# Kernel tuning notes

Hardware: AMD Instinct MI355X
Metric: run time of the kernel (lower is better)

Reference implementation:

```python
import jax, jax.numpy as jnp
import numpy as np

B, N = 4, 8192
D = 128
DEPTH = 4
LEAF = 32
HEADS = 4
HD = D // HEADS
SLOTS = 24
RANKS = [20, 32, 52, 82]                      # rank at encoder step j (fine -> coarse)
EXP = [RANKS[j] * (2 ** j) for j in range(DEPTH)]  # HODLR head output dims


def _rope_tables(seq_len, dim):
    inv_freq = 1.0 / (10000.0 ** (jnp.arange(0, dim, 2, dtype=jnp.float32) / dim))
    t = jnp.arange(seq_len, dtype=jnp.float32)
    freqs = t[:, None] * inv_freq[None, :]
    emb = jnp.concatenate([freqs, freqs], axis=-1)   # [S, dim]
    return jnp.cos(emb), jnp.sin(emb)


def _rotate_half(x):
    x1, x2 = jnp.split(x, 2, axis=-1)
    return jnp.concatenate([-x2, x1], axis=-1)


def _layernorm(x, g, b, eps=1e-5):
    mu = jnp.mean(x, -1, keepdims=True)
    var = jnp.mean((x - mu) ** 2, -1, keepdims=True)
    return (x - mu) * jax.lax.rsqrt(var + eps) * g + b


def _block_attn(h, qkv_w, qkv_b, pw, pb, cos, sin):
    Bc, Nc, C = h.shape
    nb = Nc // LEAF
    xb = h.reshape(Bc * nb, LEAF, C)
    qkv = (xb @ qkv_w + qkv_b).reshape(Bc * nb, LEAF, 3, HEADS, HD)
    qkv = qkv.transpose(2, 0, 3, 1, 4)               # [3, BN, H, L, hd]
    q, k, v = qkv[0], qkv[1], qkv[2]
    q = q * cos + _rotate_half(q) * sin              # full-dim RoPE (rope_dim == head_dim)
    k = k * cos + _rotate_half(k) * sin
    attn = jax.nn.softmax(jnp.einsum('bhqd,bhkd->bhqk', q, k) * (HD ** -0.5), axis=-1)
    o = jnp.einsum('bhqk,bhkd->bhqd', attn, v).transpose(0, 2, 1, 3).reshape(Bc * nb, LEAF, C)
    return (o @ pw + pb).reshape(Bc, Nc, C)


def _forward(x, cen_w, cen_b, nbr_w, nbr_b, inp_w, inp_b,
             leafp_w, leafp_b, leafh_w, leafh_b, log_scale_leaf,
             ln1_g, ln1_b, qkv_w, qkv_b, attnp_w, attnp_b,
             ln2_g, ln2_b, mlp1_w, mlp1_b, mlp2_w, mlp2_b, ds_w, ds_b,
             hu_w0, hu_b0, hv_w0, hv_b0, hu_w1, hu_b1, hv_w1, hv_b1,
             hu_w2, hu_b2, hv_w2, hv_b2, hu_w3, hu_b3, hv_w3, hv_b3):
    Bx, Nx, _ = x.shape
    # --- SymmetricNeighborEmbed (24 neighbor slots, vectorized) ---
    pos_i = x[..., 0:3]
    diag_i = x[..., 3:4]
    h_center = jnp.concatenate([pos_i, diag_i], -1) @ cen_w + cen_b          # [B,N,D]
    nb_feat = x[..., 4:4 + 5 * SLOTS].reshape(Bx, Nx, SLOTS, 5)
    rel = nb_feat[..., 0:1]
    pos_j = nb_feat[..., 1:4]
    w_ij = nb_feat[..., 4:5]
    active = (w_ij != 0.0).astype(x.dtype)
    feat = jnp.concatenate([rel * active, (pos_j - pos_i[:, :, None, :]) * active, w_ij], -1)
    e = (feat @ nbr_w + nbr_b) * active                                       # [B,N,24,D]
    h = h_center + jnp.sum(e, axis=2)
    h = h @ inp_w + inp_b
    # --- leaf dense diagonal blocks ---
    nl = Nx // LEAF
    hl = h.reshape(Bx, nl, LEAF, D) @ leafp_w + leafp_b                       # [B,nl,32,32]
    u_leaf = hl @ leafh_w + leafh_b
    dense = jnp.einsum('blik,bljk->blij', u_leaf, u_leaf) * jnp.exp(log_scale_leaf)
    diag_a = x[..., 3]                                                        # scale_A defaults to 1.0
    mask = jnp.abs(diag_a) > 1e-6
    new_diag = jnp.where(mask, 1.0 / jnp.where(mask, diag_a, 1.0), 1.0).reshape(Bx, nl, LEAF)
    dense = dense + new_diag[..., :, None] * jnp.eye(LEAF, dtype=x.dtype)
    # --- down-only encoder: transformer block -> HODLR head -> 2:1 downsample ---
    cos, sin = _rope_tables(LEAF, HD)
    hu = [(hu_w0, hu_b0), (hu_w1, hu_b1), (hu_w2, hu_b2), (hu_w3, hu_b3)]
    hv = [(hv_w0, hv_b0), (hv_w1, hv_b1), (hv_w2, hv_b2), (hv_w3, hv_b3)]
    us, vs = [], []
    for j in range(DEPTH):
        a = _block_attn(_layernorm(h, ln1_g[j], ln1_b[j]),
                        qkv_w[j], qkv_b[j], attnp_w[j], attnp_b[j], cos, sin)
        h = h + a
        m = _layernorm(h, ln2_g[j], ln2_b[j])
        m = jax.nn.gelu(m @ mlp1_w[j] + mlp1_b[j], approximate=False) @ mlp2_w[j] + mlp2_b[j]
        h = h + m
        us.append((h @ hu[j][0] + hu[j][1]).reshape(Bx, Nx, RANKS[j]))
        vs.append((h @ hv[j][0] + hv[j][1]).reshape(Bx, Nx, RANKS[j]))
        Bh, n, c = h.shape
        h = h.reshape(Bh, n // 2, 2 * c) @ ds_w[j] + ds_b[j]
    # single flat output: dense leaf blocks + all U/V HODLR factors
    return jnp.concatenate([dense.reshape(Bx, -1),
                            jnp.concatenate(us, -1).reshape(Bx, -1),
                            jnp.concatenate(vs, -1).reshape(Bx, -1)], -1)


def setup_inputs():
    key = jax.random.key(0)
    ks = iter(jax.random.split(key, 64))
    def rn(shape, s=0.05):
        return jax.random.normal(next(ks), shape, jnp.float32) * s
    z = lambda *s: jnp.zeros(s, jnp.float32)
    o = lambda *s: jnp.ones(s, jnp.float32)
    inp = {
        'x': jax.random.normal(next(ks), (B, N, 4 + 5 * SLOTS), jnp.float32),
        'cen_w': rn((4, D)), 'cen_b': z(D),
        'nbr_w': rn((5, D)), 'nbr_b': z(D),
        'inp_w': rn((D, D)), 'inp_b': z(D),
        'leafp_w': rn((D, LEAF)), 'leafp_b': z(LEAF),
        'leafh_w': rn((LEAF, LEAF), 0.01), 'leafh_b': z(LEAF),
        'log_scale_leaf': jnp.full((1,), np.log(0.01), jnp.float32),
        'ln1_g': o(DEPTH, D), 'ln1_b': z(DEPTH, D),
        'qkv_w': rn((DEPTH, D, 3 * D)), 'qkv_b': z(DEPTH, 3 * D),
        'attnp_w': rn((DEPTH, D, D)), 'attnp_b': z(DEPTH, D),
        'ln2_g': o(DEPTH, D), 'ln2_b': z(DEPTH, D),
        'mlp1_w': rn((DEPTH, D, 4 * D)), 'mlp1_b': z(DEPTH, 4 * D),
        'mlp2_w': rn((DEPTH, 4 * D, D)), 'mlp2_b': z(DEPTH, D),
        'ds_w': rn((DEPTH, 2 * D, D)), 'ds_b': z(DEPTH, D),
    }
    for j in range(DEPTH):
        inp['hu_w%d' % j] = rn((D, EXP[j]), 0.01)
        inp['hu_b%d' % j] = z(EXP[j])
        inp['hv_w%d' % j] = rn((D, EXP[j]), 0.01)
        inp['hv_b%d' % j] = z(EXP[j])
    return inp


def reference(x, cen_w, cen_b, nbr_w, nbr_b, inp_w, inp_b,
              leafp_w, leafp_b, leafh_w, leafh_b, log_scale_leaf,
              ln1_g, ln1_b, qkv_w, qkv_b, attnp_w, attnp_b,
              ln2_g, ln2_b, mlp1_w, mlp1_b, mlp2_w, mlp2_b, ds_w, ds_b,
              hu_w0, hu_b0, hv_w0, hv_b0, hu_w1, hu_b1, hv_w1, hv_b1,
              hu_w2, hu_b2, hv_w2, hv_b2, hu_w3, hu_b3, hv_w3, hv_b3):
    return _forward(x, cen_w, cen_b, nbr_w, nbr_b, inp_w, inp_b,
                    leafp_w, leafp_b, leafh_w, leafh_b, log_scale_leaf,
                    ln1_g, ln1_b, qkv_w, qkv_b, attnp_w, attnp_b,
                    ln2_g, ln2_b, mlp1_w, mlp1_b, mlp2_w, mlp2_b, ds_w, ds_b,
                    hu_w0, hu_b0, hv_w0, hv_b0, hu_w1, hu_b1, hv_w1, hv_b1,
                    hu_w2, hu_b2, hv_w2, hv_b2, hu_w3, hu_b3, hv_w3, hv_b3)
```

## Files before the change

### kernel.cpp

```cpp
#include <hip/hip_runtime.h>
#include <math.h>

#define DEV __device__ __forceinline__

constexpr int XFv = 124;
constexpr size_t OPB   = 3309568;
constexpr size_t UBASE = 262144;
constexpr size_t VBASE = 1785856;
constexpr int UVWID = 186;

using bfrag  = __attribute__((ext_vector_type(8))) short;
using f32x4v = __attribute__((ext_vector_type(4))) float;

DEV float* at4p(float* base, int t, int c0, int W) {
  return base + t * W + ((c0 + 4 * t) & (W - 1));
}
DEV float& at1r(float* base, int t, int c, int W) {
  return base[t * W + (((c & ~3) + 4 * t) & (W - 1)) + (c & 3)];
}
DEV float4 ld4g(const float* p) { return *(const float4*)p; }
DEV void fma4(float4& a, float s, const float4& w) {
  a.x += s * w.x; a.y += s * w.y; a.z += s * w.z; a.w += s * w.w;
}
DEV float gelu_fast(float x) {
  float x2 = x * x;
  float z = x * (1.5957691216057308f + 0.0713551f * x2);
  float e = __expf(z);
  float r = 1.0f - __frcp_rn(e + 1.0f);
  return x * r;
}
DEV ushort f2bf(float x) {
  unsigned u = __float_as_uint(x);
  unsigned r = (u + 0x7fffu + ((u >> 16) & 1u)) >> 16;
  return (ushort)r;
}
DEV void stb128(ushort* b, int row, int col, float v) {
  b[row * 128 + (((col & ~7) + 8 * row) & 127) + (col & 7)] = f2bf(v);
}

__global__ __launch_bounds__(256) void wprep_all_kernel(
    const float* __restrict__ src0, ushort* __restrict__ dst0, int K, int N) {
  size_t off = (size_t)blockIdx.z * K * N;
  const float* src = src0 + off;
  ushort* dst = dst0 + off;
  __shared__ float S[64][65];
  int tid = threadIdx.x;
  int k0 = blockIdx.x * 64, n0 = blockIdx.y * 64;
  for (int i = tid; i < 64 * 64; i += 256) {
    int kk = i >> 6, nn = i & 63;
    S[kk][nn] = src[(size_t)(k0 + kk) * N + n0 + nn];
  }
  __syncthreads();
  int n = tid >> 2, kq = tid & 3;
  unsigned pk[8];
#pragma unroll
  for (int i = 0; i < 8; i++) {
    int k = kq * 16 + 2 * i;
    pk[i] = (unsigned)f2bf(S[k][n]) | ((unsigned)f2bf(S[k + 1][n]) << 16);
  }
  unsigned* dp = (unsigned*)&dst[(size_t)(n0 + n) * K + k0 + kq * 16];
#pragma unroll
  for (int i = 0; i < 8; i++) dp[i] = pk[i];
}

struct UVDesc {
  const float* src[8];
  ushort* dst[8];
  int expj[8];
  int npad[8];
};
__global__ __launch_bounds__(256) void uvprep_all_kernel(UVDesc d) {
  int mi = blockIdx.y;
  int i = blockIdx.x * 256 + threadIdx.x;
  int expj = d.expj[mi];
  if (i >= d.npad[mi] * 128) return;
  int n = i >> 7, k = i & 127;
  d.dst[mi][(size_t)n * 128 + k] =
      (n < expj) ? f2bf(d.src[mi][(size_t)k * expj + n]) : (ushort)0;
}

__global__ __launch_bounds__(128) void weff_prep_kernel(
    const float* __restrict__ cw, const float* __restrict__ cb,
    const float* __restrict__ nw, const float* __restrict__ nb,
    const float* __restrict__ iw, const float* __restrict__ ib,
    float* __restrict__ weff, float* __restrict__ ropetab) {
  __shared__ float S[11 * 128];
  int tid = threadIdx.x;
  for (int i = tid; i < 512; i += 128) S[i] = cw[i];
  for (int i = tid; i < 640; i += 128) S[512 + i] = nw[i];
  S[1152 + tid] = nb[tid];
  S[1280 + tid] = cb[tid];
  __syncthreads();
  float acc[11];
#pragma unroll
  for (int r = 0; r < 10; r++) acc[r] = 0.f;
  acc[10] = ib[tid];
  for (int k = 0; k < 128; k++) {
    float w = iw[k * 128 + tid];
#pragma unroll
    for (int r = 0; r < 11; r++) acc[r] += S[r * 128 + k] * w;
  }
#pragma unroll
  for (int r = 0; r < 11; r++) weff[r * 128 + tid] = acc[r];
  for (int idx = tid; idx < 512; idx += 128) {
    int pos = idx >> 4, d = idx & 15;
    float ang = (float)pos * expf(-0.57564627324851148f * (float)d);
    ropetab[idx] = cosf(ang);
    ropetab[512 + idx] = sinf(ang);
  }
}

__global__ __launch_bounds__(256) void node_embed2_kernel(
    const float* __restrict__ x, const float* __restrict__ weff,
    float* __restrict__ h) {
  __shared__ float XR[64 * XFv];
  __shared__ float RF[64][11];
  __shared__ __align__(16) float WE[11 * 128];
  int tid = threadIdx.x;
  int node0 = blockIdx.x * 64;
  for (int i = tid; i < 64 * XFv; i += 256)
    XR[i] = x[(size_t)node0 * XFv + i];
  for (int i = tid; i < 11 * 128; i += 256) WE[i] = weff[i];
  __syncthreads();
  {
    int nn = tid >> 2, sl = tid & 3;
    const float* xr = XR + nn * XFv;
    float p0 = xr[0], p1 = xr[1], p2 = xr[2];
    float g[6] = {0.f, 0.f, 0.f, 0.f, 0.f, 0.f};
#pragma unroll
    for (int s = 0; s < 6; s++) {
      const float* f = xr + 4 + 5 * (sl * 6 + s);
      float w = f[4];
      if (w != 0.0f) {
        g[0] += f[0]; g[1] += f[1] - p0; g[2] += f[2] - p1;
        g[3] += f[3] - p2; g[4] += w; g[5] += 1.0f;
      }
    }
#pragma unroll
    for (int i = 0; i < 6; i++) {
      g[i] += __shfl_xor(g[i], 1);
      g[i] += __shfl_xor(g[i], 2);
    }
    if (sl == 0) {
      RF[nn][0] = p0; RF[nn][1] = p1; RF[nn][2] = p2; RF[nn][3] = xr[3];
#pragma unroll
      for (int i = 0; i < 6; i++) RF[nn][4 + i] = g[i];
    }
  }
  __syncthreads();
  {
    int w = tid >> 6, lane = tid & 63;
    int c4 = lane & 31, hi = lane >> 5;
    const float4* WE4 = (const float4*)WE;
#pragma unroll
    for (int rr = 0; rr < 8; rr++) {
      int node = w * 16 + rr * 2 + hi;
      float4 acc = WE4[10 * 32 + c4];
#pragma unroll
      for (int f = 0; f < 10; f++)
        fma4(acc, RF[node][f], WE4[f * 32 + c4]);
      *(float4*)&h[(size_t)(node0 + node) * 128 + c4 * 4] = acc;
    }
  }
}

__global__ __launch_bounds__(256) void leaf_dense_kernel(
    const float* __restrict__ h, const float* __restrict__ x,
    const float* __restrict__ lpw, const float* __restrict__ lpb,
    const float* __restrict__ lhw, const float* __restrict__ lhb,
    const float* __restrict__ lsc, float* __restrict__ out) {
  __shared__ __align__(16) float HS[32 * 128];
  __shared__ __align__(16) float HL[32 * 32];
  __shared__ __align__(16) float UL[32 * 32];
  int tid = threadIdx.x;
  int leaf = blockIdx.x;
  size_t base = (size_t)leaf * (32 * 128);
  for (int i = tid; i < 32 * 128; i += 256) {
    int t = i >> 7, c = i & 127;
    at1r(HS, t, c, 128) = h[base + i];
  }
  __syncthreads();
  int t = tid & 31, cg = tid >> 5;
  {
    float4 acc = ld4g(&lpb[4 * cg]);
    for (int k4 = 0; k4 < 128; k4 += 4) {
      float4 xv = *(const float4*)at4p(HS, t, k4, 128);
      float xa[4] = {xv.x, xv.y, xv.z, xv.w};
#pragma unroll
      for (int kk = 0; kk < 4; kk++)
        fma4(acc, xa[kk], ld4g(&lpw[(k4 + kk) * 32 + 4 * cg]));
    }
    *(float4*)at4p(HL, t, 4 * cg, 32) = acc;
  }
  __syncthreads();
  {
    float4 acc = ld4g(&lhb[4 * cg]);
    for (int k4 = 0; k4 < 32; k4 += 4) {
      float4 xv = *(const float4*)at4p(HL, t, k4, 32);
      float xa[4] = {xv.x, xv.y, xv.z, xv.w};
#pragma unroll
      for (int kk = 0; kk < 4; kk++)
        fma4(acc, xa[kk], ld4g(&lhw[(k4 + kk) * 32 + 4 * cg]));
    }
    *(float4*)at4p(UL, t, 4 * cg, 32) = acc;
  }
  __syncthreads();
  {
    float scale = expf(lsc[0]);
    float acc[4] = {0.f, 0.f, 0.f, 0.f};
    for (int k4 = 0; k4 < 32; k4 += 4) {
      float4 xv = *(const float4*)at4p(UL, t, k4, 32);
      float xa[4] = {xv.x, xv.y, xv.z, xv.w};
#pragma unroll
      for (int kk = 0; kk < 4; kk++) {
        int k = k4 + kk;
#pragma unroll
        for (int i2 = 0; i2 < 4; i2++)
          acc[i2] += xa[kk] * at1r(UL, 4 * cg + i2, k, 32);
      }
    }
    int b = leaf >> 8, l = leaf & 255;
#pragma unroll
    for (int i2 = 0; i2 < 4; i2++) {
      int c = 4 * cg + i2;
      float v = acc[i2] * scale;
      if (c == t) {
        float dg = x[(size_t)(leaf * 32 + t) * XFv + 3];
        v += (fabsf(dg) > 1e-6f) ? (1.0f / dg) : 1.0f;
      }
      out[(size_t)b * OPB + (size_t)l * 1024 + t * 32 + c] = v;
    }
  }
}

__global__ __launch_bounds__(256) void layer_mfma_kernel(
    float* __restrict__ h,
    const float* __restrict__ lng, const float* __restrict__ lnb,
    const ushort* __restrict__ wqkvt, const float* __restrict__ bqkv,
    const ushort* __restrict__ wpt, const float* __restrict__ pb,
    const float* __restrict__ rt,
    const float* __restrict__ ln2g, const float* __restrict__ ln2b,
    const ushort* __restrict__ w1t, const float* __restrict__ b1,
    const ushort* __restrict__ w2t, const float* __restrict__ b2) {
  __shared__ __align__(16) ushort SM[32768];
  ushort* XN = SM;
  ushort* QB = SM + 8192;
  ushort* KB = SM + 16384;
  ushort* VT = SM + 24576;
  float*  HS = (float*)(SM + 16384);
  int tid = threadIdx.x;
  size_t base = (size_t)blockIdx.x * (64 * 128);

  {
    int m = tid >> 2, p = tid & 3;
    const float* row = h + base + m * 128 + p * 32;
    float v[32];
    float s = 0.f;
#pragma unroll
    for (int i = 0; i < 32; i += 4) {
      float4 t4 = ld4g(row + i);
      v[i] = t4.x; v[i + 1] = t4.y; v[i + 2] = t4.z; v[i + 3] = t4.w;
      s += t4.x + t4.y + t4.z + t4.w;
    }
    s += __shfl_xor(s, 1); s += __shfl_xor(s, 2);
    float mu = s * (1.0f / 128.0f);
    float s2 = 0.f;
#pragma unroll
    for (int i = 0; i < 32; i++) { float d = v[i] - mu; s2 += d * d; }
    s2 += __shfl_xor(s2, 1); s2 += __shfl_xor(s2, 2);
    float rs = rsqrtf(s2 * (1.0f / 128.0f) + 1e-5f);
    unsigned* XW = (unsigned*)XN;
#pragma unroll
    for (int i = 0; i < 32; i += 2) {
      int c = p * 32 + i;
      float x0 = (v[i] - mu) * rs * lng[c] + lnb[c];
      float x1 = (v[i + 1] - mu) * rs * lng[c + 1] + lnb[c + 1];
      int kp = c >> 1;
      XW[m * 64 + ((kp + 4 * m) & 63)] =
          (unsigned)f2bf(x0) | ((unsigned)f2bf(x1) << 16);
    }
  }
  __syncthreads();

  int w = tid >> 6, l = tid & 63, lm = l & 15, q = l >> 4;

  {
    f32x4v acc[4][6];
#pragma unroll
    for (int mt = 0; mt < 4; mt++)
#pragma unroll
      for (int nt = 0; nt < 6; nt++) acc[mt][nt] = (f32x4v){0.f, 0.f, 0.f, 0.f};
    for (int ks = 0; ks < 4; ks++) {
      bfrag a[4];
#pragma unroll
      for (int mt = 0; mt < 4; mt++) {
        int mm = mt * 16 + lm;
        a[mt] = *(const bfrag*)&XN[mm * 128 + ((ks * 32 + q * 8 + 8 * mm) & 127)];
      }
#pragma unroll
      for (int nt = 0; nt < 6; nt++) {
        int n = w * 96 + nt * 16 + lm;
        bfrag b = *(const bfrag*)&wqkvt[(size_t)n * 128 + ks * 32 + q * 8];
#pragma unroll
        for (int mt = 0; mt < 4; mt++)
          acc[mt][nt] = __builtin_amdgcn_mfma_f32_16x16x32_bf16(
              a[mt], b, acc[mt][nt], 0, 0, 0);
      }
    }
    float csA[4] = {}, snA[4] = {}, csB[4] = {}, snB[4] = {};
    if (w < 3) {
#pragma unroll
      for (int r = 0; r < 4; r++) {
        int pa = q * 4 + r;
        csA[r] = rt[pa * 16 + lm];        snA[r] = rt[512 + pa * 16 + lm];
        csB[r] = rt[(pa + 16) * 16 + lm]; snB[r] = rt[512 + (pa + 16) * 16 + lm];
      }
    }
#pragma unroll
    for (int p2 = 0; p2 < 3; p2++) {
      int g = w * 6 + 2 * p2;
      int ne = g * 16 + lm;
      if (g < 16) {
        float be = bqkv[ne], bo = bqkv[ne + 16];
        ushort* dst = (g < 8) ? QB : KB;
        int de = (g < 8) ? ne : ne - 128;
#pragma unroll
        for (int mt = 0; mt < 4; mt++)
#pragma unroll
          for (int r = 0; r < 4; r++) {
            int mm = mt * 16 + q * 4 + r;
            float cs = (mt & 1) ? csB[r] : csA[r];
            float sn = (mt & 1) ? snB[r] : snA[r];
            float e = acc[mt][2 * p2][r] + be;
            float o = acc[mt][2 * p2 + 1][r] + bo;
            stb128(dst, mm, de, e * cs - o * sn);
            stb128(dst, mm, de + 16, o * cs + e * sn);
          }
      } else {
#pragma unroll
        for (int h2 = 0; h2 < 2; h2++) {
          int nt = 2 * p2 + h2;
          int nv = (g + h2) * 16 + lm;
          int dv = nv - 256;
          float bv = bqkv[nv];
#pragma unroll
          for (int mt = 0; mt < 4; mt++) {
            int t0 = mt * 16 + q * 4;
            short4 pk;
            pk.x = (short)f2bf(acc[mt][nt][0] + bv);
            pk.y = (short)f2bf(acc[mt][nt][1] + bv);
            pk.z = (short)f2bf(acc[mt][nt][2] + bv);
            pk.w = (short)f2bf(acc[mt][nt][3] + bv);
            *(short4*)&VT[dv * 64 + (((t0 & ~7) + 8 * dv) & 63) + (t0 & 7)] = pk;
          }
        }
      }
    }
  }
  __syncthreads();

  ushort* SP = XN;
  {
#pragma unroll
    for (int ci = 0; ci < 2; ci++) {
      int combo = w + 4 * ci;
      int head = combo >> 1, leaf = combo & 1;
      f32x4v sc[2][2];
#pragma unroll
      for (int a2 = 0; a2 < 2; a2++)
#pragma unroll
        for (int b2 = 0; b2 < 2; b2++) sc[a2][b2] = (f32x4v){0.f, 0.f, 0.f, 0.f};
      bfrag qa[2], kb[2];
#pragma unroll
      for (int mt2 = 0; mt2 < 2; mt2++) {
        int row = leaf * 32 + mt2 * 16 + lm;
        qa[mt2] = *(const bfrag*)&QB[row * 128 + ((head * 32 + q * 8 + 8 * row) & 127)];
      }
#pragma unroll
      for (int nt2 = 0; nt2 < 2; nt2++) {
        int kt = leaf * 32 + nt2 * 16 + lm;
        kb[nt2] = *(const bfrag*)&KB[kt * 128 + ((head * 32 + q * 8 + 8 * kt) & 127)];
      }
#pragma unroll
      for (int mt2 = 0; mt2 < 2; mt2++)
#pragma unroll
        for (int nt2 = 0; nt2 < 2; nt2++)
          sc[mt2][nt2] = __builtin_amdgcn_mfma_f32_16x16x32_bf16(
              qa[mt2], kb[nt2], sc[mt2][nt2], 0, 0, 0);
      const float scl = 0.17677669529663688f;
#pragma unroll
      for (int mt2 = 0; mt2 < 2; mt2++)
#pragma unroll
        for (int nt2 = 0; nt2 < 2; nt2++)
#pragma unroll
          for (int r = 0; r < 4; r++) {
            int qt = leaf * 32 + mt2 * 16 + q * 4 + r;
            int kc = nt2 * 16 + lm;
            SP[head * 2048 + qt * 32 + (((kc & ~7) + 8 * qt) & 31) + (kc & 7)] =
                f2bf(sc[mt2][nt2][r] * scl);
          }
    }
  }
  __syncthreads();

  {
    int head = tid >> 6, qt = tid & 63;
    ushort* rowp = SP + head * 2048 + qt * 32;
    float v[32];
#pragma unroll
    for (int pc = 0; pc < 4; pc++) {
      uint4 ch = *(const uint4*)&rowp[pc * 8];
      unsigned uu[4] = {ch.x, ch.y, ch.z, ch.w};
#pragma unroll
      for (int i2 = 0; i2 < 4; i2++) {
        v[pc * 8 + 2 * i2]     = __uint_as_float(uu[i2] << 16);
        v[pc * 8 + 2 * i2 + 1] = __uint_as_float(uu[i2] & 0xffff0000u);
      }
    }
    float mx = -1e30f;
#pragma unroll
    for (int i = 0; i < 32; i++) mx = fmaxf(mx, v[i]);
    float s = 0.f;
#pragma unroll
    for (int i = 0; i < 32; i++) { v[i] = __expf(v[i] - mx); s += v[i]; }
    float inv = 1.0f / s;
#pragma unroll
    for (int pc = 0; pc < 4; pc++) {
      uint4 ch;
      unsigned uu[4];
#pragma unroll
      for (int i2 = 0; i2 < 4; i2++)
        uu[i2] = (unsigned)f2bf(v[pc * 8 + 2 * i2] * inv) |
                 ((unsigned)f2bf(v[pc * 8 + 2 * i2 + 1] * inv) << 16);
      ch.x = uu[0]; ch.y = uu[1]; ch.z = uu[2]; ch.w = uu[3];
      *(uint4*)&rowp[pc * 8] = ch;
    }
  }
  __syncthreads();

  ushort* OB = QB;
  {
#pragma unroll
    for (int ci = 0; ci < 2; ci++) {
      int combo = w + 4 * ci;
      int head = combo >> 1, leaf = combo & 1;
      f32x4v ov[2][2];
#pragma unroll
      for (int a2 = 0; a2 < 2; a2++)
#pragma unroll
        for (int b2 = 0; b2 < 2; b2++) ov[a2][b2] = (f32x4v){0.f, 0.f, 0.f, 0.f};
      bfrag pa[2], vb[2];
#pragma unroll
      for (int mt2 = 0; mt2 < 2; mt2++) {
        int qt = leaf * 32 + mt2 * 16 + lm;
        pa[mt2] = *(const bfrag*)&SP[head * 2048 + qt * 32 + ((q * 8 + 8 * qt) & 31)];
      }
#pragma unroll
      for (int nt2 = 0; nt2 < 2; nt2++) {
        int gdim = head * 32 + nt2 * 16 + lm;
        int t0 = leaf * 32 + q * 8;
        vb[nt2] = *(const bfrag*)&VT[gdim * 64 + ((t0 + 8 * gdim) & 63)];
      }
#pragma unroll
      for (int mt2 = 0; mt2 < 2; mt2++)
#pragma unroll
        for (int nt2 = 0; nt2 < 2; nt2++)
          ov[mt2][nt2] = __builtin_amdgcn_mfma_f32_16x16x32_bf16(
              pa[mt2], vb[nt2], ov[mt2][nt2], 0, 0, 0);
#pragma unroll
      for (int mt2 = 0; mt2 < 2; mt2++)
#pragma unroll
        for (int nt2 = 0; nt2 < 2; nt2++)
#pragma unroll
          for (int r = 0; r < 4; r++) {
            int qt = leaf * 32 + mt2 * 16 + q * 4 + r;
            int gdim = head * 32 + nt2 * 16 + lm;
            stb128(OB, qt, gdim, ov[mt2][nt2][r]);
          }
    }
  }
  __syncthreads();

  {
    f32x4v po[4][2];
#pragma unroll
    for (int mt = 0; mt < 4; mt++)
#pragma unroll
      for (int nt = 0; nt < 2; nt++) po[mt][nt] = (f32x4v){0.f, 0.f, 0.f, 0.f};
    for (int ks = 0; ks < 4; ks++) {
      bfrag a[4];
#pragma unroll
      for (int mt = 0; mt < 4; mt++) {
        int mm = mt * 16 + lm;
        a[mt] = *(const bfrag*)&OB[mm * 128 + ((ks * 32 + q * 8 + 8 * mm) & 127)];
      }
#pragma unroll
      for (int nt = 0; nt < 2; nt++) {
        int n = w * 32 + nt * 16 + lm;
        bfrag b = *(const bfrag*)&wpt[(size_t)n * 128 + ks * 32 + q * 8];
#pragma unroll
        for (int mt = 0; mt < 4; mt++)
          po[mt][nt] = __builtin_amdgcn_mfma_f32_16x16x32_bf16(
              a[mt], b, po[mt][nt], 0, 0, 0);
      }
    }
#pragma unroll
    for (int nt = 0; nt < 2; nt++) {
      int n = w * 32 + nt * 16 + lm;
      float bv = pb[n];
#pragma unroll
      for (int mt = 0; mt < 4; mt++)
#pragma unroll
        for (int r = 0; r < 4; r++) {
          int mm = mt * 16 + q * 4 + r;
          HS[mm * 128 + n] = po[mt][nt][r] + bv;
        }
    }
  }
  __syncthreads();

  {
    int j = tid & 31;
    int c0 = j * 4;
    float g0 = ln2g[c0], g1 = ln2g[c0 + 1], g2 = ln2g[c0 + 2], g3 = ln2g[c0 + 3];
    float e0 = ln2b[c0], e1 = ln2b[c0 + 1], e2 = ln2b[c0 + 2], e3 = ln2b[c0 + 3];
    unsigned* XW = (unsigned*)XN;
#pragma unroll
    for (int k2 = 0; k2 < 8; k2++) {
      int idx = tid + 256 * k2;
      int tok = idx >> 5;
      float4 hg = ld4g(&h[base + (size_t)idx * 4]);
      float4 ao = *(const float4*)&HS[idx * 4];
      float4 hn;
      hn.x = hg.x + ao.x; hn.y = hg.y + ao.y;
      hn.z = hg.z + ao.z; hn.w = hg.w + ao.w;
      *(float4*)&HS[idx * 4] = hn;
      float s = hn.x + hn.y + hn.z + hn.w;
      s += __shfl_xor(s, 1); s += __shfl_xor(s, 2); s += __shfl_xor(s, 4);
      s += __shfl_xor(s, 8); s += __shfl_xor(s, 16);
      float mu = s * (1.0f / 128.0f);
      float d0 = hn.x - mu, d1 = hn.y - mu, d2 = hn.z - mu, d3 = hn.w - mu;
      float s2 = d0 * d0 + d1 * d1 + d2 * d2 + d3 * d3;
      s2 += __shfl_xor(s2, 1); s2 += __shfl_xor(s2, 2); s2 += __shfl_xor(s2, 4);
      s2 += __shfl_xor(s2, 8); s2 += __shfl_xor(s2, 16);
      float rs = rsqrtf(s2 * (1.0f / 128.0f) + 1e-5f);
      float x0 = d0 * rs * g0 + e0;
      float x1 = d1 * rs * g1 + e1;
      float x2 = d2 * rs * g2 + e2;
      float x3 = d3 * rs * g3 + e3;
      int kp = 2 * j;
      XW[tok * 64 + ((kp + 4 * tok) & 63)] =
          (unsigned)f2bf(x0) | ((unsigned)f2bf(x1) << 16);
      XW[tok * 64 + ((kp + 1 + 4 * tok) & 63)] =
          (unsigned)f2bf(x2) | ((unsigned)f2bf(x3) << 16);
    }
  }
  __syncthreads();

  ushort* HC = QB;
  f32x4v acc2[4][2];
#pragma unroll
  for (int mt = 0; mt < 4; mt++)
#pragma unroll
    for (int nt = 0; nt < 2; nt++) acc2[mt][nt] = (f32x4v){0.f, 0.f, 0.f, 0.f};

  for (int hc = 0; hc < 4; hc++) {
    f32x4v acc1[4][2];
#pragma unroll
    for (int mt = 0; mt < 4; mt++)
#pragma unroll
      for (int nt = 0; nt < 2; nt++) acc1[mt][nt] = (f32x4v){0.f, 0.f, 0.f, 0.f};
#pragma unroll
    for (int ks = 0; ks < 4; ks++) {
      bfrag a[4];
#pragma unroll
      for (int mt = 0; mt < 4; mt++) {
        int mm = mt * 16 + lm;
        a[mt] = *(const bfrag*)&XN[mm * 128 + ((ks * 32 + q * 8 + 8 * mm) & 127)];
      }
#pragma unroll
      for (int nt = 0; nt < 2; nt++) {
        int n = hc * 128 + w * 32 + nt * 16 + lm;
        bfrag b = *(const bfrag*)&w1t[(size_t)n * 128 + ks * 32 + q * 8];
#pragma unroll
        for (int mt = 0; mt < 4; mt++)
          acc1[mt][nt] = __builtin_amdgcn_mfma_f32_16x16x32_bf16(
              a[mt], b, acc1[mt][nt], 0, 0, 0);
      }
    }
    if (hc) __syncthreads();
#pragma unroll
    for (int nt = 0; nt < 2; nt++) {
      int nl = w * 32 + nt * 16 + lm;
      float b1v = b1[hc * 128 + nl];
#pragma unroll
      for (int mt = 0; mt < 4; mt++)
#pragma unroll
        for (int r = 0; r < 4; r++) {
          int mm = mt * 16 + q * 4 + r;
          float val = gelu_fast(acc1[mt][nt][r] + b1v);
          HC[mm * 128 + (((nl & ~7) + 8 * mm) & 127) + (nl & 7)] = f2bf(val);
        }
    }
    __syncthreads();
#pragma unroll
    for (int ks = 0; ks < 4; ks++) {
      bfrag a[4];
#pragma unroll
      for (int mt = 0; mt < 4; mt++) {
        int mm = mt * 16 + lm;
        a[mt] = *(const bfrag*)&HC[mm * 128 + ((ks * 32 + q * 8 + 8 * mm) & 127)];
      }
#pragma unroll
      for (int nt = 0; nt < 2; nt++) {
        int n = w * 32 + nt * 16 + lm;
        bfrag b = *(const bfrag*)&w2t[(size_t)n * 512 + hc * 128 + ks * 32 + q * 8];
#pragma unroll
        for (int mt = 0; mt < 4; mt++)
          acc2[mt][nt] = __builtin_amdgcn_mfma_f32_16x16x32_bf16(
              a[mt], b, acc2[mt][nt], 0, 0, 0);
      }
    }
  }

#pragma unroll
  for (int nt = 0; nt < 2; nt++) {
    int n = w * 32 + nt * 16 + lm;
    float b2v = b2[n];
#pragma unroll
    for (int mt = 0; mt < 4; mt++)
#pragma unroll
      for (int r = 0; r < 4; r++) {
        int mm = mt * 16 + q * 4 + r;
        h[base + (size_t)mm * 128 + n] = HS[mm * 128 + n] + acc2[mt][nt][r] + b2v;
      }
  }
}

template <int EXPJ, int RANK, int LVL, int NSPLIT>
__global__ __launch_bounds__(256) void uv_mfma_kernel(
    const float* __restrict__ h,
    const ushort* __restrict__ uwt, const float* __restrict__ ub,
    const ushort* __restrict__ vwt, const float* __restrict__ vb,
    float* __restrict__ out, int Nj) {
  constexpr int NT16 = (EXPJ + 15) / 16;
  constexpr int NJOBS = 2 * NT16;
  constexpr int COFF = (LVL == 0) ? 0 : (LVL == 1) ? 20 : (LVL == 2) ? 52 : 104;
  __shared__ __align__(16) ushort XN[64 * 128];
  int tid = threadIdx.x;
  int t0 = blockIdx.x * 64;
  size_t base = (size_t)t0 * 128;
  {
    int m = tid >> 2, p = tid & 3;
    const float* row = h + base + m * 128 + p * 32;
    unsigned* XW = (unsigned*)XN;
#pragma unroll
    for (int i = 0; i < 32; i += 4) {
      float4 t4 = ld4g(row + i);
      int kp = (p * 32 + i) >> 1;
      XW[m * 64 + ((kp + 4 * m) & 63)] =
          (unsigned)f2bf(t4.x) | ((unsigned)f2bf(t4.y) << 16);
      XW[m * 64 + ((kp + 1 + 4 * m) & 63)] =
          (unsigned)f2bf(t4.z) | ((unsigned)f2bf(t4.w) << 16);
    }
  }
  __syncthreads();
  int bidx = t0 / Nj;
  int tl0 = t0 - bidx * Nj;
  size_t obase = (size_t)bidx * OPB;
  int w = tid >> 6, l = tid & 63, lm = l & 15, q = l >> 4;
  int gw = w + 4 * blockIdx.y;
  for (int jj = gw; jj < NJOBS; jj += 4 * NSPLIT) {
    int uvsel = jj & 1, nt = jj >> 1;
    const ushort* wt = uvsel ? vwt : uwt;
    const float* bias = uvsel ? vb : ub;
    size_t ob = obase + (uvsel ? VBASE : UBASE);
    f32x4v acc[4];
#pragma unroll
    for (int mt = 0; mt < 4; mt++) acc[mt] = (f32x4v){0.f, 0.f, 0.f, 0.f};
    for (int ks = 0; ks < 4; ks++) {
      bfrag b = *(const bfrag*)&wt[(size_t)(nt * 16 + lm) * 128 + ks * 32 + q * 8];
#pragma unroll
      for (int mt = 0; mt < 4; mt++) {
        int mm = mt * 16 + lm;
        int ke = ks * 32 + q * 8;
        bfrag a = *(const bfrag*)&XN[mm * 128 + ((ke + 8 * mm) & 127)];
        acc[mt] = __builtin_amdgcn_mfma_f32_16x16x32_bf16(a, b, acc[mt], 0, 0, 0);
      }
    }
    int c = nt * 16 + lm;
    if (c < EXPJ) {
      float bv = bias[c];
      int cdiv = c / RANK, cmod = c - cdiv * RANK;
#pragma unroll
      for (int mt = 0; mt < 4; mt++)
#pragma unroll
        for (int r = 0; r < 4; r++) {
          int mm = mt * 16 + q * 4 + r;
          int nrow = ((tl0 + mm) << LVL) + cdiv;
          out[ob + (size_t)nrow * UVWID + COFF + cmod] = acc[mt][r] + bv;
        }
    }
  }
}

__global__ __launch_bounds__(256) void ds_mfma_kernel(
    const float* __restrict__ hin, float* __restrict__ hout,
    const ushort* __restrict__ wt, const float* __restrict__ bias) {
  __shared__ __align__(16) ushort XN[64 * 256];
  int tid = threadIdx.x;
  size_t base = (size_t)blockIdx.x * (64 * 256);
  {
    int m = tid >> 2, p = tid & 3;
    const float* row = hin + base + m * 256 + p * 64;
    unsigned* XW = (unsigned*)XN;
#pragma unroll
    for (int i = 0; i < 64; i += 4) {
      float4 t4 = ld4g(row + i);
      int kp = (p * 64 + i) >> 1;
      XW[m * 128 + ((kp + 4 * m) & 127)] =
          (unsigned)f2bf(t4.x) | ((unsigned)f2bf(t4.y) << 16);
      XW[m * 128 + ((kp + 1 + 4 * m) & 127)] =
          (unsigned)f2bf(t4.z) | ((unsigned)f2bf(t4.w) << 16);
    }
  }
  __syncthreads();
  int w = tid >> 6, l = tid & 63, lm = l & 15, q = l >> 4;
  f32x4v acc[4][2];
#pragma unroll
  for (int mt = 0; mt < 4; mt++)
#pragma unroll
    for (int nt = 0; nt < 2; nt++) acc[mt][nt] = (f32x4v){0.f, 0.f, 0.f, 0.f};
  for (int ks = 0; ks < 8; ks++) {
    bfrag a[4];
#pragma unroll
    for (int mt = 0; mt < 4; mt++) {
      int mm = mt * 16 + lm;
      a[mt] = *(const bfrag*)&XN[mm * 256 + ((ks * 32 + q * 8 + 8 * mm) & 255)];
    }
#pragma unroll
    for (int nt = 0; nt < 2; nt++) {
      int n = w * 32 + nt * 16 + lm;
      bfrag b = *(const bfrag*)&wt[(size_t)n * 256 + ks * 32 + q * 8];
#pragma unroll
      for (int mt = 0; mt < 4; mt++)
        acc[mt][nt] = __builtin_amdgcn_mfma_f32_16x16x32_bf16(
            a[mt], b, acc[mt][nt], 0, 0, 0);
    }
  }
  size_t obase = (size_t)blockIdx.x * (64 * 128);
#pragma unroll
  for (int nt = 0; nt < 2; nt++) {
    int n = w * 32 + nt * 16 + lm;
    float bv = bias[n];
#pragma unroll
    for (int mt = 0; mt < 4; mt++)
#pragma unroll
      for (int r = 0; r < 4; r++) {
        int mm = mt * 16 + q * 4 + r;
        hout[obase + (size_t)mm * 128 + n] = acc[mt][nt][r] + bv;
      }
  }
}

extern "C" void kernel_launch(void* const* d_in, const int* in_sizes, int n_in,
                              void* d_out, int out_size, void* d_ws, size_t ws_size,
                              hipStream_t stream) {
  const float* x       = (const float*)d_in[0];
  const float* cen_w   = (const float*)d_in[1];
  const float* cen_b   = (const float*)d_in[2];
  const float* nbr_w   = (const float*)d_in[3];
  const float* nbr_b   = (const float*)d_in[4];
  const float* inp_w   = (const float*)d_in[5];
  const float* inp_b   = (const float*)d_in[6];
  const float* leafp_w = (const float*)d_in[7];
  const float* leafp_b = (const float*)d_in[8];
  const float* leafh_w = (const float*)d_in[9];
  const float* leafh_b = (const float*)d_in[10];
  const float* lscale  = (const float*)d_in[11];
  const float* ln1_g   = (const float*)d_in[12];
  const float* ln1_b   = (const float*)d_in[13];
  const float* qkv_w   = (const float*)d_in[14];
  const float* qkv_b   = (const float*)d_in[15];
  const float* attnp_w = (const float*)d_in[16];
  const float* attnp_b = (const float*)d_in[17];
  const float* ln2_g   = (const float*)d_in[18];
  const float* ln2_b   = (const float*)d_in[19];
  const float* mlp1_w  = (const float*)d_in[20];
  const float* mlp1_b  = (const float*)d_in[21];
  const float* mlp2_w  = (const float*)d_in[22];
  const float* mlp2_b  = (const float*)d_in[23];
  const float* ds_w    = (const float*)d_in[24];
  const float* ds_b    = (const float*)d_in[25];
  const float* huw[4], *hub[4], *hvw[4], *hvb[4];
  for (int j = 0; j < 4; j++) {
    huw[j] = (const float*)d_in[26 + 4 * j];
    hub[j] = (const float*)d_in[27 + 4 * j];
    hvw[j] = (const float*)d_in[28 + 4 * j];
    hvb[j] = (const float*)d_in[29 + 4 * j];
  }
  float* out = (float*)d_out;
  float* hA = (float*)d_ws;
  float* hB = hA + (size_t)4 * 8192 * 128;
  ushort* w1t = (ushort*)(hB + (size_t)2097152);
  ushort* w2t = w1t + (size_t)4 * 65536;
  ushort* uvt = w2t + (size_t)4 * 65536;
  const int NPAD[4] = {32, 64, 208, 656};
  ushort* uwt[4]; ushort* vwt[4];
  ushort* p = uvt;
  for (int j = 0; j < 4; j++) {
    uwt[j] = p; p += (size_t)NPAD[j] * 128;
    vwt[j] = p; p += (size_t)NPAD[j] * 128;
  }
  ushort* wqkvt = p;
  ushort* wpt   = wqkvt + (size_t)4 * 384 * 128;
  ushort* dswt  = wpt + (size_t)4 * 128 * 128;
  float* weff   = (float*)(dswt + (size_t)4 * 128 * 256);
  float* ropetab = weff + 1408;
  const int EXPJ_[4] = {20, 64, 208, 656};

  weff_prep_kernel<<<1, 128, 0, stream>>>(
      cen_w, cen_b, nbr_w, nbr_b, inp_w, inp_b, weff, ropetab);
  wprep_all_kernel<<<dim3(2, 8, 4), 256, 0, stream>>>(mlp1_w, w1t, 128, 512);
  wprep_all_kernel<<<dim3(8, 2, 4), 256, 0, stream>>>(mlp2_w, w2t, 512, 128);
  wprep_all_kernel<<<dim3(2, 6, 4), 256, 0, stream>>>(qkv_w, wqkvt, 128, 384);
  wprep_all_kernel<<<dim3(2, 2, 4), 256, 0, stream>>>(attnp_w, wpt, 128, 128);
  wprep_all_kernel<<<dim3(4, 2, 4), 256, 0, stream>>>(ds_w, dswt, 256, 128);
  {
    UVDesc d;
    for (int j = 0; j < 4; j++) {
      d.src[2 * j] = huw[j];     d.dst[2 * j] = uwt[j];
      d.src[2 * j + 1] = hvw[j]; d.dst[2 * j + 1] = vwt[j];
      d.expj[2 * j] = EXPJ_[j];  d.expj[2 * j + 1] = EXPJ_[j];
      d.npad[2 * j] = NPAD[j];   d.npad[2 * j + 1] = NPAD[j];
    }
    uvprep_all_kernel<<<dim3(328, 8), 256, 0, stream>>>(d);
  }

  node_embed2_kernel<<<(4 * 8192) / 64, 256, 0, stream>>>(x, weff, hA);
  leaf_dense_kernel<<<(4 * 8192) / 32, 256, 0, stream>>>(
      hA, x, leafp_w, leafp_b, leafh_w, leafh_b, lscale, out);

  float* cur = hA;
  float* nxt = hB;
  int Nj = 8192;
  for (int j = 0; j < 4; j++) {
    int tokens = 4 * Nj;
    layer_mfma_kernel<<<tokens / 64, 256, 0, stream>>>(
        cur, ln1_g + j * 128, ln1_b + j * 128,
        wqkvt + (size_t)j * 49152, qkv_b + j * 384,
        wpt + (size_t)j * 16384, attnp_b + j * 128, ropetab,
        ln2_g + j * 128, ln2_b + j * 128,
        w1t + (size_t)j * 65536, mlp1_b + j * 512,
        w2t + (size_t)j * 65536, mlp2_b + j * 128);
    if (j == 0)
      uv_mfma_kernel<20, 20, 0, 1><<<dim3(tokens / 64, 1), 256, 0, stream>>>(
          cur, uwt[0], hub[0], vwt[0], hvb[0], out, Nj);
    else if (j == 1)
      uv_mfma_kernel<64, 32, 1, 2><<<dim3(tokens / 64, 2), 256, 0, stream>>>(
          cur, uwt[1], hub[1], vwt[1], hvb[1], out, Nj);
    else if (j == 2)
      uv_mfma_kernel<208, 52, 2, 4><<<dim3(tokens / 64, 4), 256, 0, stream>>>(
          cur, uwt[2], hub[2], vwt[2], hvb[2], out, Nj);
    else
      uv_mfma_kernel<656, 82, 3, 8><<<dim3(tokens / 64, 8), 256, 0, stream>>>(
          cur, uwt[3], hub[3], vwt[3], hvb[3], out, Nj);
    ds_mfma_kernel<<<tokens / 128, 256, 0, stream>>>(
        cur, nxt, dswt + (size_t)j * 32768, ds_b + j * 128);
    float* tmp = cur; cur = nxt; nxt = tmp;
    Nj >>= 1;
  }
  (void)in_sizes; (void)n_in; (void)out_size; (void)ws_size;
}
```

Measured before the change: 470.4 us.

## Shrink layer kernel tile to 32 tokens per block for higher occupancy

Each layer_mfma_kernel block now processes one 32-token leaf instead of two, halving shared memory (64KB to 32KB) and accumulator registers, and requests 4 blocks per CU via launch bounds. Attention is remapped so each wave handles one head of the single leaf, and only half the threads run the softmax. The HS fp32 scratch now uses a swizzled layout to reduce LDS bank conflicts. In exchange, weight fragments are reloaded from global/L2 twice as often per token, and the grid doubles.

```diff
diff --git a/kernel.cpp b/kernel.cpp
--- a/kernel.cpp
+++ b/kernel.cpp
@@ -233,7 +233,7 @@
   }
 }
 
-__global__ __launch_bounds__(256) void layer_mfma_kernel(
+__global__ __launch_bounds__(256, 4) void layer_mfma_kernel(
     float* __restrict__ h,
     const float* __restrict__ lng, const float* __restrict__ lnb,
     const ushort* __restrict__ wqkvt, const float* __restrict__ bqkv,
@@ -242,37 +242,37 @@
     const float* __restrict__ ln2g, const float* __restrict__ ln2b,
     const ushort* __restrict__ w1t, const float* __restrict__ b1,
     const ushort* __restrict__ w2t, const float* __restrict__ b2) {
-  __shared__ __align__(16) ushort SM[32768];
+  __shared__ __align__(16) ushort SM[16384];
   ushort* XN = SM;
-  ushort* QB = SM + 8192;
-  ushort* KB = SM + 16384;
-  ushort* VT = SM + 24576;
-  float*  HS = (float*)(SM + 16384);
+  ushort* QB = SM + 4096;
+  ushort* KB = SM + 8192;
+  ushort* VT = SM + 12288;
+  float*  HS = (float*)(SM + 8192);
   int tid = threadIdx.x;
-  size_t base = (size_t)blockIdx.x * (64 * 128);
-
-  {
-    int m = tid >> 2, p = tid & 3;
-    const float* row = h + base + m * 128 + p * 32;
-    float v[32];
+  size_t base = (size_t)blockIdx.x * (32 * 128);
+
+  {
+    int m = tid >> 3, p = tid & 7;
+    const float* row = h + base + m * 128 + p * 16;
+    float v[16];
     float s = 0.f;
 #pragma unroll
-    for (int i = 0; i < 32; i += 4) {
+    for (int i = 0; i < 16; i += 4) {
       float4 t4 = ld4g(row + i);
       v[i] = t4.x; v[i + 1] = t4.y; v[i + 2] = t4.z; v[i + 3] = t4.w;
       s += t4.x + t4.y + t4.z + t4.w;
     }
-    s += __shfl_xor(s, 1); s += __shfl_xor(s, 2);
+    s += __shfl_xor(s, 1); s += __shfl_xor(s, 2); s += __shfl_xor(s, 4);
     float mu = s * (1.0f / 128.0f);
     float s2 = 0.f;
 #pragma unroll
-    for (int i = 0; i < 32; i++) { float d = v[i] - mu; s2 += d * d; }
-    s2 += __shfl_xor(s2, 1); s2 += __shfl_xor(s2, 2);
+    for (int i = 0; i < 16; i++) { float d = v[i] - mu; s2 += d * d; }
+    s2 += __shfl_xor(s2, 1); s2 += __shfl_xor(s2, 2); s2 += __shfl_xor(s2, 4);
     float rs = rsqrtf(s2 * (1.0f / 128.0f) + 1e-5f);
     unsigned* XW = (unsigned*)XN;
 #pragma unroll
-    for (int i = 0; i < 32; i += 2) {
-      int c = p * 32 + i;
+    for (int i = 0; i < 16; i += 2) {
+      int c = p * 16 + i;
       float x0 = (v[i] - mu) * rs * lng[c] + lnb[c];
       float x1 = (v[i + 1] - mu) * rs * lng[c + 1] + lnb[c + 1];
       int kp = c >> 1;
@@ -285,15 +285,15 @@
   int w = tid >> 6, l = tid & 63, lm = l & 15, q = l >> 4;
 
   {
-    f32x4v acc[4][6];
-#pragma unroll
-    for (int mt = 0; mt < 4; mt++)
+    f32x4v acc[2][6];
+#pragma unroll
+    for (int mt = 0; mt < 2; mt++)
 #pragma unroll
       for (int nt = 0; nt < 6; nt++) acc[mt][nt] = (f32x4v){0.f, 0.f, 0.f, 0.f};
     for (int ks = 0; ks < 4; ks++) {
-      bfrag a[4];
-#pragma unroll
-      for (int mt = 0; mt < 4; mt++) {
+      bfrag a[2];
+#pragma unroll
+      for (int mt = 0; mt < 2; mt++) {
         int mm = mt * 16 + lm;
         a[mt] = *(const bfrag*)&XN[mm * 128 + ((ks * 32 + q * 8 + 8 * mm) & 127)];
       }
@@ -302,7 +302,7 @@
         int n = w * 96 + nt * 16 + lm;
         bfrag b = *(const bfrag*)&wqkvt[(size_t)n * 128 + ks * 32 + q * 8];
 #pragma unroll
-        for (int mt = 0; mt < 4; mt++)
+        for (int mt = 0; mt < 2; mt++)
           acc[mt][nt] = __builtin_amdgcn_mfma_f32_16x16x32_bf16(
               a[mt], b, acc[mt][nt], 0, 0, 0);
       }
@@ -325,7 +325,7 @@
         ushort* dst = (g < 8) ? QB : KB;
         int de = (g < 8) ? ne : ne - 128;
 #pragma unroll
-        for (int mt = 0; mt < 4; mt++)
+        for (int mt = 0; mt < 2; mt++)
 #pragma unroll
           for (int r = 0; r < 4; r++) {
             int mm = mt * 16 + q * 4 + r;
@@ -344,14 +344,14 @@
           int dv = nv - 256;
           float bv = bqkv[nv];
 #pragma unroll
-          for (int mt = 0; mt < 4; mt++) {
+          for (int mt = 0; mt < 2; mt++) {
             int t0 = mt * 16 + q * 4;
             short4 pk;
             pk.x = (short)f2bf(acc[mt][nt][0] + bv);
             pk.y = (short)f2bf(acc[mt][nt][1] + bv);
             pk.z = (short)f2bf(acc[mt][nt][2] + bv);
             pk.w = (short)f2bf(acc[mt][nt][3] + bv);
-            *(short4*)&VT[dv * 64 + (((t0 & ~7) + 8 * dv) & 63) + (t0 & 7)] = pk;
+            *(short4*)&VT[dv * 32 + (((t0 & ~7) + 8 * dv) & 31) + (t0 & 7)] = pk;
           }
         }
       }
@@ -361,136 +361,129 @@
 
   ushort* SP = XN;
   {
-#pragma unroll
-    for (int ci = 0; ci < 2; ci++) {
-      int combo = w + 4 * ci;
-      int head = combo >> 1, leaf = combo & 1;
-      f32x4v sc[2][2];
-#pragma unroll
-      for (int a2 = 0; a2 < 2; a2++)
-#pragma unroll
-        for (int b2 = 0; b2 < 2; b2++) sc[a2][b2] = (f32x4v){0.f, 0.f, 0.f, 0.f};
-      bfrag qa[2], kb[2];
-#pragma unroll
-      for (int mt2 = 0; mt2 < 2; mt2++) {
-        int row = leaf * 32 + mt2 * 16 + lm;
-        qa[mt2] = *(const bfrag*)&QB[row * 128 + ((head * 32 + q * 8 + 8 * row) & 127)];
-      }
-#pragma unroll
-      for (int nt2 = 0; nt2 < 2; nt2++) {
-        int kt = leaf * 32 + nt2 * 16 + lm;
-        kb[nt2] = *(const bfrag*)&KB[kt * 128 + ((head * 32 + q * 8 + 8 * kt) & 127)];
-      }
-#pragma unroll
-      for (int mt2 = 0; mt2 < 2; mt2++)
-#pragma unroll
-        for (int nt2 = 0; nt2 < 2; nt2++)
-          sc[mt2][nt2] = __builtin_amdgcn_mfma_f32_16x16x32_bf16(
-              qa[mt2], kb[nt2], sc[mt2][nt2], 0, 0, 0);
-      const float scl = 0.17677669529663688f;
-#pragma unroll
-      for (int mt2 = 0; mt2 < 2; mt2++)
-#pragma unroll
-        for (int nt2 = 0; nt2 < 2; nt2++)
-#pragma unroll
-          for (int r = 0; r < 4; r++) {
-            int qt = leaf * 32 + mt2 * 16 + q * 4 + r;
-            int kc = nt2 * 16 + lm;
-            SP[head * 2048 + qt * 32 + (((kc & ~7) + 8 * qt) & 31) + (kc & 7)] =
-                f2bf(sc[mt2][nt2][r] * scl);
-          }
-    }
-  }
-  __syncthreads();
-
-  {
-    int head = tid >> 6, qt = tid & 63;
-    ushort* rowp = SP + head * 2048 + qt * 32;
-    float v[32];
-#pragma unroll
-    for (int pc = 0; pc < 4; pc++) {
-      uint4 ch = *(const uint4*)&rowp[pc * 8];
-      unsigned uu[4] = {ch.x, ch.y, ch.z, ch.w};
-#pragma unroll
-      for (int i2 = 0; i2 < 4; i2++) {
-        v[pc * 8 + 2 * i2]     = __uint_as_float(uu[i2] << 16);
-        v[pc * 8 + 2 * i2 + 1] = __uint_as_float(uu[i2] & 0xffff0000u);
-      }
-    }
-    float mx = -1e30f;
-#pragma unroll
-    for (int i = 0; i < 32; i++) mx = fmaxf(mx, v[i]);
-    float s = 0.f;
-#pragma unroll
-    for (int i = 0; i < 32; i++) { v[i] = __expf(v[i] - mx); s += v[i]; }
-    float inv = 1.0f / s;
-#pragma unroll
-    for (int pc = 0; pc < 4; pc++) {
-      uint4 ch;
-      unsigned uu[4];
-#pragma unroll
-      for (int i2 = 0; i2 < 4; i2++)
-        uu[i2] = (unsigned)f2bf(v[pc * 8 + 2 * i2] * inv) |
-                 ((unsigned)f2bf(v[pc * 8 + 2 * i2 + 1] * inv) << 16);
-      ch.x = uu[0]; ch.y = uu[1]; ch.z = uu[2]; ch.w = uu[3];
-      *(uint4*)&rowp[pc * 8] = ch;
+    int head = w;
+    f32x4v sc[2][2];
+#pragma unroll
+    for (int a2 = 0; a2 < 2; a2++)
+#pragma unroll
+      for (int b2 = 0; b2 < 2; b2++) sc[a2][b2] = (f32x4v){0.f, 0.f, 0.f, 0.f};
+    bfrag qa[2], kb[2];
+#pragma unroll
+    for (int mt2 = 0; mt2 < 2; mt2++) {
+      int row = mt2 * 16 + lm;
+      qa[mt2] = *(const bfrag*)&QB[row * 128 + ((head * 32 + q * 8 + 8 * row) & 127)];
+    }
+#pragma unroll
+    for (int nt2 = 0; nt2 < 2; nt2++) {
+      int kt = nt2 * 16 + lm;
+      kb[nt2] = *(const bfrag*)&KB[kt * 128 + ((head * 32 + q * 8 + 8 * kt) & 127)];
+    }
+#pragma unroll
+    for (int mt2 = 0; mt2 < 2; mt2++)
+#pragma unroll
+      for (int nt2 = 0; nt2 < 2; nt2++)
+        sc[mt2][nt2] = __builtin_amdgcn_mfma_f32_16x16x32_bf16(
+            qa[mt2], kb[nt2], sc[mt2][nt2], 0, 0, 0);
+    const float scl = 0.17677669529663688f;
+#pragma unroll
+    for (int mt2 = 0; mt2 < 2; mt2++)
+#pragma unroll
+      for (int nt2 = 0; nt2 < 2; nt2++)
+#pragma unroll
+        for (int r = 0; r < 4; r++) {
+          int qt = mt2 * 16 + q * 4 + r;
+          int kc = nt2 * 16 + lm;
+          SP[head * 1024 + qt * 32 + (((kc & ~7) + 8 * qt) & 31) + (kc & 7)] =
+              f2bf(sc[mt2][nt2][r] * scl);
+        }
+  }
+  __syncthreads();
+
+  {
+    if (tid < 128) {
+      int head = tid >> 5, qt = tid & 31;
+      ushort* rowp = SP + head * 1024 + qt * 32;
+      float v[32];
+#pragma unroll
+      for (int pc = 0; pc < 4; pc++) {
+        uint4 ch = *(const uint4*)&rowp[pc * 8];
+        unsigned uu[4] = {ch.x, ch.y, ch.z, ch.w};
+#pragma unroll
+        for (int i2 = 0; i2 < 4; i2++) {
+          v[pc * 8 + 2 * i2]     = __uint_as_float(uu[i2] << 16);
+          v[pc * 8 + 2 * i2 + 1] = __uint_as_float(uu[i2] & 0xffff0000u);
+        }
+      }
+      float mx = -1e30f;
+#pragma unroll
+      for (int i = 0; i < 32; i++) mx = fmaxf(mx, v[i]);
+      float s = 0.f;
+#pragma unroll
+      for (int i = 0; i < 32; i++) { v[i] = __expf(v[i] - mx); s += v[i]; }
+      float inv = 1.0f / s;
+#pragma unroll
+      for (int pc = 0; pc < 4; pc++) {
+        uint4 ch;
+        unsigned uu[4];
+#pragma unroll
+        for (int i2 = 0; i2 < 4; i2++)
+          uu[i2] = (unsigned)f2bf(v[pc * 8 + 2 * i2] * inv) |
+                   ((unsigned)f2bf(v[pc * 8 + 2 * i2 + 1] * inv) << 16);
+        ch.x = uu[0]; ch.y = uu[1]; ch.z = uu[2]; ch.w = uu[3];
+        *(uint4*)&rowp[pc * 8] = ch;
+      }
     }
   }
   __syncthreads();
 
   ushort* OB = QB;
   {
-#pragma unroll
-    for (int ci = 0; ci < 2; ci++) {
-      int combo = w + 4 * ci;
-      int head = combo >> 1, leaf = combo & 1;
-      f32x4v ov[2][2];
-#pragma unroll
-      for (int a2 = 0; a2 < 2; a2++)
-#pragma unroll
-        for (int b2 = 0; b2 < 2; b2++) ov[a2][b2] = (f32x4v){0.f, 0.f, 0.f, 0.f};
-      bfrag pa[2], vb[2];
-#pragma unroll
-      for (int mt2 = 0; mt2 < 2; mt2++) {
-        int qt = leaf * 32 + mt2 * 16 + lm;
-        pa[mt2] = *(const bfrag*)&SP[head * 2048 + qt * 32 + ((q * 8 + 8 * qt) & 31)];
-      }
-#pragma unroll
-      for (int nt2 = 0; nt2 < 2; nt2++) {
-        int gdim = head * 32 + nt2 * 16 + lm;
-        int t0 = leaf * 32 + q * 8;
-        vb[nt2] = *(const bfrag*)&VT[gdim * 64 + ((t0 + 8 * gdim) & 63)];
-      }
-#pragma unroll
-      for (int mt2 = 0; mt2 < 2; mt2++)
-#pragma unroll
-        for (int nt2 = 0; nt2 < 2; nt2++)
-          ov[mt2][nt2] = __builtin_amdgcn_mfma_f32_16x16x32_bf16(
-              pa[mt2], vb[nt2], ov[mt2][nt2], 0, 0, 0);
-#pragma unroll
-      for (int mt2 = 0; mt2 < 2; mt2++)
-#pragma unroll
-        for (int nt2 = 0; nt2 < 2; nt2++)
-#pragma unroll
-          for (int r = 0; r < 4; r++) {
-            int qt = leaf * 32 + mt2 * 16 + q * 4 + r;
-            int gdim = head * 32 + nt2 * 16 + lm;
-            stb128(OB, qt, gdim, ov[mt2][nt2][r]);
-          }
-    }
-  }
-  __syncthreads();
-
-  {
-    f32x4v po[4][2];
-#pragma unroll
-    for (int mt = 0; mt < 4; mt++)
+    int head = w;
+    f32x4v ov[2][2];
+#pragma unroll
+    for (int a2 = 0; a2 < 2; a2++)
+#pragma unroll
+      for (int b2 = 0; b2 < 2; b2++) ov[a2][b2] = (f32x4v){0.f, 0.f, 0.f, 0.f};
+    bfrag pa[2], vb[2];
+#pragma unroll
+    for (int mt2 = 0; mt2 < 2; mt2++) {
+      int qt = mt2 * 16 + lm;
+      pa[mt2] = *(const bfrag*)&SP[head * 1024 + qt * 32 + ((q * 8 + 8 * qt) & 31)];
+    }
+#pragma unroll
+    for (int nt2 = 0; nt2 < 2; nt2++) {
+      int gdim = head * 32 + nt2 * 16 + lm;
+      vb[nt2] = *(const bfrag*)&VT[gdim * 32 + ((q * 8 + 8 * gdim) & 31)];
+    }
+#pragma unroll
+    for (int mt2 = 0; mt2 < 2; mt2++)
+#pragma unroll
+      for (int nt2 = 0; nt2 < 2; nt2++)
+        ov[mt2][nt2] = __builtin_amdgcn_mfma_f32_16x16x32_bf16(
+            pa[mt2], vb[nt2], ov[mt2][nt2], 0, 0, 0);
+#pragma unroll
+    for (int mt2 = 0; mt2 < 2; mt2++)
+#pragma unroll
+      for (int nt2 = 0; nt2 < 2; nt2++)
+#pragma unroll
+        for (int r = 0; r < 4; r++) {
+          int qt = mt2 * 16 + q * 4 + r;
+          int gdim = head * 32 + nt2 * 16 + lm;
+          stb128(OB, qt, gdim, ov[mt2][nt2][r]);
+        }
+  }
+  __syncthreads();
+
+  {
+    f32x4v po[2][2];
+#pragma unroll
+    for (int mt = 0; mt < 2; mt++)
 #pragma unroll
       for (int nt = 0; nt < 2; nt++) po[mt][nt] = (f32x4v){0.f, 0.f, 0.f, 0.f};
     for (int ks = 0; ks < 4; ks++) {
-      bfrag a[4];
-#pragma unroll
-      for (int mt = 0; mt < 4; mt++) {
+      bfrag a[2];
+#pragma unroll
+      for (int mt = 0; mt < 2; mt++) {
         int mm = mt * 16 + lm;
         a[mt] = *(const bfrag*)&OB[mm * 128 + ((ks * 32 + q * 8 + 8 * mm) & 127)];
       }
@@ -499,7 +492,7 @@
         int n = w * 32 + nt * 16 + lm;
         bfrag b = *(const bfrag*)&wpt[(size_t)n * 128 + ks * 32 + q * 8];
 #pragma unroll
-        for (int mt = 0; mt < 4; mt++)
+        for (int mt = 0; mt < 2; mt++)
           po[mt][nt] = __builtin_amdgcn_mfma_f32_16x16x32_bf16(
               a[mt], b, po[mt][nt], 0, 0, 0);
       }
@@ -509,11 +502,11 @@
       int n = w * 32 + nt * 16 + lm;
       float bv = pb[n];
 #pragma unroll
-      for (int mt = 0; mt < 4; mt++)
+      for (int mt = 0; mt < 2; mt++)
 #pragma unroll
         for (int r = 0; r < 4; r++) {
           int mm = mt * 16 + q * 4 + r;
-          HS[mm * 128 + n] = po[mt][nt][r] + bv;
+          at1r(HS, mm, n, 128) = po[mt][nt][r] + bv;
         }
     }
   }
@@ -526,15 +519,15 @@
     float e0 = ln2b[c0], e1 = ln2b[c0 + 1], e2 = ln2b[c0 + 2], e3 = ln2b[c0 + 3];
     unsigned* XW = (unsigned*)XN;
 #pragma unroll
-    for (int k2 = 0; k2 < 8; k2++) {
+    for (int k2 = 0; k2 < 4; k2++) {
       int idx = tid + 256 * k2;
       int tok = idx >> 5;
       float4 hg = ld4g(&h[base + (size_t)idx * 4]);
-      float4 ao = *(const float4*)&HS[idx * 4];
+      float4 ao = *(const float4*)at4p(HS, tok, 4 * j, 128);
       float4 hn;
       hn.x = hg.x + ao.x; hn.y = hg.y + ao.y;
       hn.z = hg.z + ao.z; hn.w = hg.w + ao.w;
-      *(float4*)&HS[idx * 4] = hn;
+      *(float4*)at4p(HS, tok, 4 * j, 128) = hn;
       float s = hn.x + hn.y + hn.z + hn.w;
       s += __shfl_xor(s, 1); s += __shfl_xor(s, 2); s += __shfl_xor(s, 4);
       s += __shfl_xor(s, 8); s += __shfl_xor(s, 16);
@@ -558,23 +551,23 @@
   __syncthreads();
 
   ushort* HC = QB;
-  f32x4v acc2[4][2];
-#pragma unroll
-  for (int mt = 0; mt < 4; mt++)
+  f32x4v acc2[2][2];
+#pragma unroll
+  for (int mt = 0; mt < 2; mt++)
 #pragma unroll
     for (int nt = 0; nt < 2; nt++) acc2[mt][nt] = (f32x4v){0.f, 0.f, 0.f, 0.f};
 
   for (int hc = 0; hc < 4; hc++) {
-    f32x4v acc1[4][2];
-#pragma unroll
-    for (int mt = 0; mt < 4; mt++)
+    f32x4v acc1[2][2];
+#pragma unroll
+    for (int mt = 0; mt < 2; mt++)
 #pragma unroll
       for (int nt = 0; nt < 2; nt++) acc1[mt][nt] = (f32x4v){0.f, 0.f, 0.f, 0.f};
 #pragma unroll
     for (int ks = 0; ks < 4; ks++) {
-      bfrag a[4];
-#pragma unroll
-      for (int mt = 0; mt < 4; mt++) {
+      bfrag a[2];
+#pragma unroll
+      for (int mt = 0; mt < 2; mt++) {
         int mm = mt * 16 + lm;
         a[mt] = *(const bfrag*)&XN[mm * 128 + ((ks * 32 + q * 8 + 8 * mm) & 127)];
       }
@@ -583,7 +576,7 @@
         int n = hc * 128 + w * 32 + nt * 16 + lm;
         bfrag b = *(const bfrag*)&w1t[(size_t)n * 128 + ks * 32 + q * 8];
 #pragma unroll
-        for (int mt = 0; mt < 4; mt++)
+        for (int mt = 0; mt < 2; mt++)
           acc1[mt][nt] = __builtin_amdgcn_mfma_f32_16x16x32_bf16(
               a[mt], b, acc1[mt][nt], 0, 0, 0);
       }
@@ -594,7 +587,7 @@
       int nl = w * 32 + nt * 16 + lm;
       float b1v = b1[hc * 128 + nl];
 #pragma unroll
-      for (int mt = 0; mt < 4; mt++)
+      for (int mt = 0; mt < 2; mt++)
 #pragma unroll
         for (int r = 0; r < 4; r++) {
           int mm = mt * 16 + q * 4 + r;
@@ -605,9 +598,9 @@
     __syncthreads();
 #pragma unroll
     for (int ks = 0; ks < 4; ks++) {
-      bfrag a[4];
-#pragma unroll
-      for (int mt = 0; mt < 4; mt++) {
+      bfrag a[2];
+#pragma unroll
+      for (int mt = 0; mt < 2; mt++) {
         int mm = mt * 16 + lm;
         a[mt] = *(const bfrag*)&HC[mm * 128 + ((ks * 32 + q * 8 + 8 * mm) & 127)];
       }
@@ -616,7 +609,7 @@
         int n = w * 32 + nt * 16 + lm;
         bfrag b = *(const bfrag*)&w2t[(size_t)n * 512 + hc * 128 + ks * 32 + q * 8];
 #pragma unroll
-        for (int mt = 0; mt < 4; mt++)
+        for (int mt = 0; mt < 2; mt++)
           acc2[mt][nt] = __builtin_amdgcn_mfma_f32_16x16x32_bf16(
               a[mt], b, acc2[mt][nt], 0, 0, 0);
       }
@@ -628,11 +621,11 @@
     int n = w * 32 + nt * 16 + lm;
     float b2v = b2[n];
 #pragma unroll
-    for (int mt = 0; mt < 4; mt++)
+    for (int mt = 0; mt < 2; mt++)
 #pragma unroll
       for (int r = 0; r < 4; r++) {
         int mm = mt * 16 + q * 4 + r;
-        h[base + (size_t)mm * 128 + n] = HS[mm * 128 + n] + acc2[mt][nt][r] + b2v;
+        h[base + (size_t)mm * 128 + n] = at1r(HS, mm, n, 128) + acc2[mt][nt][r] + b2v;
       }
   }
 }
@@ -846,7 +839,7 @@
   int Nj = 8192;
   for (int j = 0; j < 4; j++) {
     int tokens = 4 * Nj;
-    layer_mfma_kernel<<<tokens / 64, 256, 0, stream>>>(
+    layer_mfma_kernel<<<tokens / 32, 256, 0, stream>>>(
         cur, ln1_g + j * 128, ln1_b + j * 128,
         wqkvt + (size_t)j * 49152, qkv_b + j * 384,
         wpt + (size_t)j * 16384, attnp_b + j * 128, ropetab,
```

Result: faster. 444.2 us (-5.6%).
